# Kernel optimization log

Hardware: AMD Instinct MI355X
Metric: run time of the kernel (lower is better)

Reference implementation:

```python
import jax, jax.numpy as jnp
import numpy as np

D = 256; NH = 8; NL = 4; NP = 4; DFF = 1024
SHAPES = [(100, 100), (50, 50), (25, 25), (13, 13)]
B = 4


def layer_norm(x, g, b, eps=1e-5):
    m = x.mean(-1, keepdims=True)
    v = ((x - m) ** 2).mean(-1, keepdims=True)
    return (x - m) * jax.lax.rsqrt(v + eps) * g + b


def setup_inputs() -> dict:
    key = jax.random.key(0)
    ks = jax.random.split(key, 12)
    Lin = sum(h * w for h, w in SHAPES)  # 13294
    w = lambda k, s: jax.random.normal(k, s, jnp.float32) * 0.02
    return dict(
        src=jax.random.normal(ks[0], (B, Lin, D), jnp.float32),
        pos=0.1 * jax.random.normal(ks[1], (B, Lin, D), jnp.float32),
        reference_points=jax.random.uniform(ks[2], (B, Lin, NL, 2), dtype=jnp.float32),
        spatial_shapes=jnp.array(SHAPES, jnp.int32),
        level_start_index=jnp.array(np.cumsum([0] + [h * w for h, w in SHAPES])[:-1], jnp.int32),
        value_w=w(ks[3], (D, D)), value_b=jnp.zeros((D,), jnp.float32),
        offs_w=w(ks[4], (D, NH * NL * NP * 2)),
        offs_b=0.5 * jax.random.normal(ks[5], (NH * NL * NP * 2,), jnp.float32),
        attn_w=w(ks[6], (D, NH * NL * NP)), attn_b=jnp.zeros((NH * NL * NP,), jnp.float32),
        out_w=w(ks[7], (D, D)), out_b=jnp.zeros((D,), jnp.float32),
        ln1_g=jnp.ones((D,), jnp.float32), ln1_b=jnp.zeros((D,), jnp.float32),
        ff1_w=w(ks[8], (D, DFF)), ff1_b=jnp.zeros((DFF,), jnp.float32),
        ff2_w=w(ks[9], (DFF, D)), ff2_b=jnp.zeros((D,), jnp.float32),
        ln2_g=jnp.ones((D,), jnp.float32), ln2_b=jnp.zeros((D,), jnp.float32),
    )


def msda(query, value_in, ref, shapes, starts, value_w, value_b, offs_w, offs_b,
         attn_w, attn_b, out_w, out_b):
    Bq, Lq, Dm = query.shape
    dh = Dm // NH
    shapes_np = np.asarray(shapes); starts_np = np.asarray(starts)
    value = (value_in @ value_w + value_b).reshape(Bq, -1, NH, dh)
    offs = (query @ offs_w + offs_b).reshape(Bq, Lq, NH, NL, NP, 2)
    aw = jax.nn.softmax((query @ attn_w + attn_b).reshape(Bq, Lq, NH, NL * NP), axis=-1)
    aw = aw.reshape(Bq, Lq, NH, NL, NP)
    # offset normalizer is (W, H) per level
    normalizer = jnp.stack([shapes[:, 1], shapes[:, 0]], -1).astype(jnp.float32)
    loc = ref[:, :, None, :, None, :] + offs / normalizer[None, None, None, :, None, :]
    out = jnp.zeros((Bq, NH, Lq, dh), jnp.float32)
    for l in range(NL):
        Hl, Wl = int(shapes_np[l, 0]), int(shapes_np[l, 1])
        s = int(starts_np[l])
        v = value[:, s:s + Hl * Wl].transpose(0, 2, 1, 3)  # [B,h,HW,dh]
        x = loc[:, :, :, l, :, 0] * Wl - 0.5  # [B,Lq,h,P], align_corners=False
        y = loc[:, :, :, l, :, 1] * Hl - 0.5
        x0 = jnp.floor(x); y0 = jnp.floor(y)
        dx = x - x0; dy = y - y0
        x0i = x0.astype(jnp.int32); y0i = y0.astype(jnp.int32)
        def gather(ix, iy):
            valid = (ix >= 0) & (ix < Wl) & (iy >= 0) & (iy < Hl)  # zero padding
            idx = jnp.clip(iy, 0, Hl - 1) * Wl + jnp.clip(ix, 0, Wl - 1)
            idx = idx.transpose(0, 2, 1, 3).reshape(Bq, NH, Lq * NP)
            g = jnp.take_along_axis(v, idx[..., None], axis=2).reshape(Bq, NH, Lq, NP, dh)
            return g * valid.transpose(0, 2, 1, 3)[..., None]
        dxh = dx.transpose(0, 2, 1, 3)[..., None]
        dyh = dy.transpose(0, 2, 1, 3)[..., None]
        sampled = (gather(x0i, y0i) * (1 - dxh) * (1 - dyh)
                   + gather(x0i + 1, y0i) * dxh * (1 - dyh)
                   + gather(x0i, y0i + 1) * (1 - dxh) * dyh
                   + gather(x0i + 1, y0i + 1) * dxh * dyh)  # [B,h,Lq,P,dh]
        awl = aw[:, :, :, l].transpose(0, 2, 1, 3)[..., None]  # [B,h,Lq,P,1]
        out = out + (sampled * awl).sum(3)
    out = out.transpose(0, 2, 1, 3).reshape(Bq, Lq, Dm)
    return out @ out_w + out_b


def reference(src, pos, reference_points, spatial_shapes, level_start_index,
              value_w, value_b, offs_w, offs_b, attn_w, attn_b, out_w, out_b,
              ln1_g, ln1_b, ff1_w, ff1_b, ff2_w, ff2_b, ln2_g, ln2_b):
    # src = with_pos_embed(src, pos): NOTE this module uses (src + pos) as BOTH query and value
    q = src + pos
    src2 = msda(q, q, reference_points, spatial_shapes, level_start_index,
                value_w, value_b, offs_w, offs_b, attn_w, attn_b, out_w, out_b)
    x = layer_norm(q + src2, ln1_g, ln1_b)  # dropout is identity at eval
    ff = jnp.maximum(x @ ff1_w + ff1_b, 0.0) @ ff2_w + ff2_b
    return layer_norm(x + ff, ln2_g, ln2_b)
```

## Files before the change

kernel.cpp:

```cpp
#include <hip/hip_runtime.h>
#include <hip/hip_bf16.h>

#define B_    4
#define LIN   13294
#define M_    (B_*LIN)
#define D_    256
#define NH_   8
#define NL_   4
#define NP_   4
#define DFF_  1024

typedef __bf16 bf16;
typedef __attribute__((ext_vector_type(8))) __bf16 bfrag8;
typedef __attribute__((ext_vector_type(4))) __bf16 bf16x4;
typedef __attribute__((ext_vector_type(4))) float facc4;

__global__ __launch_bounds__(256) void make_q(const float* __restrict__ src,
                                              const float* __restrict__ pos,
                                              float* __restrict__ q,
                                              bf16* __restrict__ qb, int n4) {
  int i = blockIdx.x * 256 + threadIdx.x;
  if (i >= n4) return;
  float4 s = ((const float4*)src)[i];
  float4 p = ((const float4*)pos)[i];
  float4 v = {s.x + p.x, s.y + p.y, s.z + p.z, s.w + p.w};
  ((float4*)q)[i] = v;
  bf16 t4[4] = {(bf16)v.x, (bf16)v.y, (bf16)v.z, (bf16)v.w};
  ((uint2*)qb)[i] = *(uint2*)t4;
}

__global__ __launch_bounds__(256) void prep_weights(
    const float* __restrict__ vw, const float* __restrict__ ow,
    const float* __restrict__ aw, const float* __restrict__ outw,
    const float* __restrict__ f1w, const float* __restrict__ f2w,
    const float* __restrict__ ob, const float* __restrict__ ab,
    bf16* __restrict__ vwt, bf16* __restrict__ oawt, bf16* __restrict__ outwt,
    bf16* __restrict__ f1wt, bf16* __restrict__ f2wt, float* __restrict__ oabias) {
  int seg = blockIdx.y;
  int idx = blockIdx.x * 256 + threadIdx.x;
  if (seg == 6) {
    if (idx < 256) oabias[idx] = ob[idx];
    else if (idx < 384) oabias[idx] = ab[idx - 256];
    return;
  }
  const float* W; bf16* Wt; int K, N;
  switch (seg) {
    case 0: W = vw;   Wt = vwt;          K = 256;  N = 256;  break;
    case 1: W = ow;   Wt = oawt;         K = 256;  N = 256;  break;
    case 2: W = aw;   Wt = oawt + 65536; K = 256;  N = 128;  break;
    case 3: W = outw; Wt = outwt;        K = 256;  N = 256;  break;
    case 4: W = f1w;  Wt = f1wt;         K = 256;  N = 1024; break;
    default: W = f2w; Wt = f2wt;         K = 1024; N = 256;  break;
  }
  if (idx < K * N) {
    int n = idx / K, k = idx - n * K;
    Wt[idx] = (bf16)W[k * N + n];
  }
}

template<bool RELU>
__global__ __launch_bounds__(256) void gemm_kernel(
    const bf16* __restrict__ A, const bf16* __restrict__ Bt,
    const float* __restrict__ bias, bf16* __restrict__ C,
    int Mdim, int K, int N) {
  __shared__ __align__(16) bf16 As[64][72];
  __shared__ __align__(16) bf16 Bs[64][72];
  int m0 = blockIdx.x * 64;
  int n0 = blockIdx.y * 64;
  int t = threadIdx.x;
  int wave = t >> 6, lane = t & 63;
  int ln = lane & 15, quad = lane >> 4;

  facc4 acc[4];
  facc4 z = {0.f, 0.f, 0.f, 0.f};
  for (int r = 0; r < 4; r++) acc[r] = z;

  for (int k0 = 0; k0 < K; k0 += 64) {
    __syncthreads();
    #pragma unroll
    for (int i = 0; i < 2; i++) {
      int idx = t + i * 256;
      int row = idx >> 3, kc = (idx & 7) * 8;
      int ag = min(m0 + row, Mdim - 1);
      *(uint4*)&As[row][kc] = *(const uint4*)&A[(size_t)ag * K + k0 + kc];
      *(uint4*)&Bs[row][kc] = *(const uint4*)&Bt[(size_t)(n0 + row) * K + k0 + kc];
    }
    __syncthreads();
    #pragma unroll
    for (int kk = 0; kk < 64; kk += 32) {
      bfrag8 bfr = *(const bfrag8*)&Bs[16 * wave + ln][kk + quad * 8];
      #pragma unroll
      for (int r = 0; r < 4; r++) {
        bfrag8 afr = *(const bfrag8*)&As[r * 16 + ln][kk + quad * 8];
        acc[r] = __builtin_amdgcn_mfma_f32_16x16x32_bf16(afr, bfr, acc[r], 0, 0, 0);
      }
    }
  }
  int col = n0 + wave * 16 + ln;
  float bv = bias[col];
  #pragma unroll
  for (int r = 0; r < 4; r++) {
    #pragma unroll
    for (int reg = 0; reg < 4; reg++) {
      int row = m0 + r * 16 + quad * 4 + reg;
      if (row < Mdim) {
        float v = acc[r][reg] + bv;
        if (RELU) v = fmaxf(v, 0.f);
        C[(size_t)row * N + col] = (bf16)v;
      }
    }
  }
}

__global__ __launch_bounds__(256) void msda_sample(
    const bf16* __restrict__ value,
    const bf16* __restrict__ OA,
    const float* __restrict__ ref,
    bf16* __restrict__ sampled) {
  int gw = (blockIdx.x * 256 + threadIdx.x) >> 6;
  int lane = threadIdx.x & 63;
  int m = gw >> 3, h = gw & 7;
  if (m >= M_) return;
  int b = m / LIN;
  int p = lane >> 2, cg = lane & 3;
  int l = p >> 2, pt = p & 3;
  int Wl = (l == 0) ? 100 : (l == 1) ? 50 : (l == 2) ? 25 : 13;
  int Hl = Wl;
  int st = (l == 0) ? 0 : (l == 1) ? 10000 : (l == 2) ? 12500 : 13125;

  float logit = (float)OA[(size_t)m * 384 + 256 + h * 16 + p];
  float mx = logit;
  #pragma unroll
  for (int msk = 4; msk < 64; msk <<= 1) mx = fmaxf(mx, __shfl_xor(mx, msk));
  float e = __expf(logit - mx);
  float se = e;
  #pragma unroll
  for (int msk = 4; msk < 64; msk <<= 1) se += __shfl_xor(se, msk);
  float w = e / se;

  float rx = ref[((size_t)m * 4 + l) * 2 + 0];
  float ry = ref[((size_t)m * 4 + l) * 2 + 1];
  float ox = (float)OA[(size_t)m * 384 + ((h * 4 + l) * 4 + pt) * 2 + 0];
  float oy = (float)OA[(size_t)m * 384 + ((h * 4 + l) * 4 + pt) * 2 + 1];
  float x = rx * (float)Wl + ox - 0.5f;
  float y = ry * (float)Hl + oy - 0.5f;
  float x0f = floorf(x), y0f = floorf(y);
  float dx = x - x0f, dy = y - y0f;
  int x0 = (int)x0f, y0 = (int)y0f;

  float acc[8];
  #pragma unroll
  for (int j = 0; j < 8; j++) acc[j] = 0.f;

  size_t vbase = ((size_t)(b * LIN + st)) * 256 + h * 32 + cg * 8;
  #pragma unroll
  for (int c = 0; c < 4; c++) {
    int cx = c & 1, cy = c >> 1;
    int xi = x0 + cx, yi = y0 + cy;
    bool valid = (xi >= 0) && (xi < Wl) && (yi >= 0) && (yi < Hl);
    int xc = min(max(xi, 0), Wl - 1);
    int yc = min(max(yi, 0), Hl - 1);
    float cw = (cx ? dx : 1.f - dx) * (cy ? dy : 1.f - dy);
    cw = valid ? cw : 0.f;
    bfrag8 vv = *(const bfrag8*)(value + vbase + (size_t)(yc * Wl + xc) * 256);
    #pragma unroll
    for (int j = 0; j < 8; j++) acc[j] += cw * (float)vv[j];
  }
  #pragma unroll
  for (int j = 0; j < 8; j++) acc[j] *= w;
  #pragma unroll
  for (int msk = 4; msk < 64; msk <<= 1) {
    #pragma unroll
    for (int j = 0; j < 8; j++) acc[j] += __shfl_xor(acc[j], msk);
  }
  if (p == 0) {
    bf16 o8[8];
    #pragma unroll
    for (int j = 0; j < 8; j++) o8[j] = (bf16)acc[j];
    *(uint4*)(sampled + (size_t)m * 256 + h * 32 + cg * 8) = *(uint4*)o8;
  }
}

__device__ inline float4 load4f(const float* p) { return *(const float4*)p; }
__device__ inline float4 load4f(const bf16* p) {
  bf16x4 v = *(const bf16x4*)p;
  float4 r = {(float)v[0], (float)v[1], (float)v[2], (float)v[3]};
  return r;
}
template<typename RT>
__global__ __launch_bounds__(256) void ln_kernel(
    const bf16* __restrict__ a, const RT* __restrict__ res,
    const float* __restrict__ g, const float* __restrict__ beta,
    float* __restrict__ out_f, bf16* __restrict__ out_b, int Mdim) {
  int wave = threadIdx.x >> 6, lane = threadIdx.x & 63;
  int row = blockIdx.x * 4 + wave;
  if (row >= Mdim) return;
  size_t base = (size_t)row * 256 + lane * 4;
  float4 av = load4f(a + base);
  float4 rv = load4f(res + base);
  float4 v = {av.x + rv.x, av.y + rv.y, av.z + rv.z, av.w + rv.w};
  float s = v.x + v.y + v.z + v.w;
  #pragma unroll
  for (int msk = 1; msk < 64; msk <<= 1) s += __shfl_xor(s, msk);
  float mean = s * (1.f / 256.f);
  float4 d = {v.x - mean, v.y - mean, v.z - mean, v.w - mean};
  float sq = d.x * d.x + d.y * d.y + d.z * d.z + d.w * d.w;
  #pragma unroll
  for (int msk = 1; msk < 64; msk <<= 1) sq += __shfl_xor(sq, msk);
  float inv = rsqrtf(sq * (1.f / 256.f) + 1e-5f);
  float4 gv = *(const float4*)(g + lane * 4);
  float4 bv = *(const float4*)(beta + lane * 4);
  float4 y = {d.x * inv * gv.x + bv.x, d.y * inv * gv.y + bv.y,
              d.z * inv * gv.z + bv.z, d.w * inv * gv.w + bv.w};
  if (out_f) *(float4*)(out_f + base) = y;
  if (out_b) {
    bf16 t4[4] = {(bf16)y.x, (bf16)y.y, (bf16)y.z, (bf16)y.w};
    *(uint2*)(out_b + base) = *(uint2*)t4;
  }
}

extern "C" void kernel_launch(void* const* d_in, const int* in_sizes, int n_in,
                              void* d_out, int out_size, void* d_ws, size_t ws_size,
                              hipStream_t stream) {
  const float* src     = (const float*)d_in[0];
  const float* pos     = (const float*)d_in[1];
  const float* refpts  = (const float*)d_in[2];
  const float* value_w = (const float*)d_in[5];
  const float* value_b = (const float*)d_in[6];
  const float* offs_w  = (const float*)d_in[7];
  const float* offs_b  = (const float*)d_in[8];
  const float* attn_w  = (const float*)d_in[9];
  const float* attn_b  = (const float*)d_in[10];
  const float* out_w   = (const float*)d_in[11];
  const float* out_b   = (const float*)d_in[12];
  const float* ln1_g   = (const float*)d_in[13];
  const float* ln1_b   = (const float*)d_in[14];
  const float* ff1_w   = (const float*)d_in[15];
  const float* ff1_b   = (const float*)d_in[16];
  const float* ff2_w   = (const float*)d_in[17];
  const float* ff2_b   = (const float*)d_in[18];
  const float* ln2_g   = (const float*)d_in[19];
  const float* ln2_b   = (const float*)d_in[20];

  char* ws = (char*)d_ws;
  size_t off = 0;
  auto take = [&](size_t bytes) -> char* {
    char* pp = ws + off;
    off += (bytes + 255) & ~(size_t)255;
    return pp;
  };
  float* q      = (float*)take((size_t)M_ * 256 * 4);
  size_t szQB   = (size_t)M_ * 256 * 2;
  size_t szOA   = (size_t)M_ * 384 * 2;
  char* R       = take(szQB * 3 + szOA);
  bf16* qb      = (bf16*)R;
  bf16* valueb  = (bf16*)(R + szQB);
  bf16* OA      = (bf16*)(R + 2 * szQB);
  bf16* sampled = (bf16*)(R + 2 * szQB + szOA);
  bf16* hb      = (bf16*)R;
  bf16* tmp     = (bf16*)take(szQB);
  bf16* x       = (bf16*)take(szQB);
  bf16* vwt     = (bf16*)take(65536 * 2);
  bf16* oawt    = (bf16*)take(98304 * 2);
  bf16* outwt   = (bf16*)take(65536 * 2);
  bf16* f1wt    = (bf16*)take(262144 * 2);
  bf16* f2wt    = (bf16*)take(262144 * 2);
  float* oabias = (float*)take(384 * 4);
  (void)ws_size; (void)in_sizes; (void)n_in; (void)out_size;

  int n4 = M_ * 256 / 4;
  make_q<<<dim3((n4 + 255) / 256), dim3(256), 0, stream>>>(src, pos, q, qb, n4);
  prep_weights<<<dim3(1024, 7), dim3(256), 0, stream>>>(
      value_w, offs_w, attn_w, out_w, ff1_w, ff2_w, offs_b, attn_b,
      vwt, oawt, outwt, f1wt, f2wt, oabias);

  dim3 blk(256);
  int mt = (M_ + 63) / 64;
  gemm_kernel<false><<<dim3(mt, 4), blk, 0, stream>>>(qb, vwt, value_b, valueb, M_, 256, 256);
  gemm_kernel<false><<<dim3(mt, 6), blk, 0, stream>>>(qb, oawt, oabias, OA, M_, 256, 384);
  msda_sample<<<dim3(M_ * 2), blk, 0, stream>>>(valueb, OA, refpts, sampled);
  gemm_kernel<false><<<dim3(mt, 4), blk, 0, stream>>>(sampled, outwt, out_b, tmp, M_, 256, 256);
  ln_kernel<float><<<dim3((M_ + 3) / 4), blk, 0, stream>>>(tmp, q, ln1_g, ln1_b, nullptr, x, M_);
  gemm_kernel<true><<<dim3(mt, 16), blk, 0, stream>>>(x, f1wt, ff1_b, hb, M_, 256, 1024);
  gemm_kernel<false><<<dim3(mt, 4), blk, 0, stream>>>(hb, f2wt, ff2_b, tmp, M_, 1024, 256);
  ln_kernel<bf16><<<dim3((M_ + 3) / 4), blk, 0, stream>>>(tmp, x, ln2_g, ln2_b, (float*)d_out, nullptr, M_);
}
```

Measured before the change: 661.3 us.

## Use 128x128 GEMM tiles with direct-to-LDS loads and rework MSDA reduction

```diff
diff --git a/kernel.cpp b/kernel.cpp
--- a/kernel.cpp
+++ b/kernel.cpp
@@ -11,9 +11,11 @@
 #define DFF_  1024
 
 typedef __bf16 bf16;
+typedef unsigned int uint;
 typedef __attribute__((ext_vector_type(8))) __bf16 bfrag8;
 typedef __attribute__((ext_vector_type(4))) __bf16 bf16x4;
 typedef __attribute__((ext_vector_type(4))) float facc4;
+typedef __attribute__((ext_vector_type(2))) float f32x2;
 
 __global__ __launch_bounds__(256) void make_q(const float* __restrict__ src,
                                               const float* __restrict__ pos,
@@ -58,55 +60,95 @@
   }
 }
 
+__device__ __forceinline__ void gload16(const void* g, void* l) {
+  __builtin_amdgcn_global_load_lds(
+      (const __attribute__((address_space(1))) uint*)g,
+      (__attribute__((address_space(3))) uint*)l, 16, 0, 0);
+}
+
 template<bool RELU>
-__global__ __launch_bounds__(256) void gemm_kernel(
+__global__ __launch_bounds__(256) void gemm128(
     const bf16* __restrict__ A, const bf16* __restrict__ Bt,
     const float* __restrict__ bias, bf16* __restrict__ C,
     int Mdim, int K, int N) {
-  __shared__ __align__(16) bf16 As[64][72];
-  __shared__ __align__(16) bf16 Bs[64][72];
-  int m0 = blockIdx.x * 64;
-  int n0 = blockIdx.y * 64;
-  int t = threadIdx.x;
-  int wave = t >> 6, lane = t & 63;
-  int ln = lane & 15, quad = lane >> 4;
-
-  facc4 acc[4];
+  __shared__ __align__(16) bf16 As[128 * 64];
+  __shared__ __align__(16) bf16 Bs[128 * 64];
+  const int t = threadIdx.x, wave = t >> 6, lane = t & 63;
+  const int m0 = blockIdx.x * 128, n0 = blockIdx.y * 128;
+  const int wr = wave >> 1, wc = wave & 1;
+  const int ln = lane & 15, quad = lane >> 4;
+  const int sr = lane >> 3, cc = lane & 7;
+  const int gcol = (cc ^ sr) * 8;
+
+  const bf16* aptr[4]; const bf16* bptr[4];
+  bf16* alds[4]; bf16* blds[4];
+  #pragma unroll
+  for (int ii = 0; ii < 4; ii++) {
+    int i = wave * 4 + ii;
+    int arow = min(m0 + i * 8 + sr, Mdim - 1);
+    aptr[ii] = A + (size_t)arow * K + gcol;
+    bptr[ii] = Bt + (size_t)(n0 + i * 8 + sr) * K + gcol;
+    alds[ii] = As + i * 512;
+    blds[ii] = Bs + i * 512;
+  }
+  int a_off[2][4], b_off[2][4];
+  #pragma unroll
+  for (int ks = 0; ks < 2; ks++) {
+    int gc = ks * 4 + quad;
+    #pragma unroll
+    for (int rt = 0; rt < 4; rt++) {
+      int ra = wr * 64 + rt * 16 + ln;
+      int rb = wc * 64 + rt * 16 + ln;
+      a_off[ks][rt] = ra * 128 + ((gc ^ (ra & 7)) * 16);
+      b_off[ks][rt] = rb * 128 + ((gc ^ (rb & 7)) * 16);
+    }
+  }
+
+  facc4 acc[4][4];
   facc4 z = {0.f, 0.f, 0.f, 0.f};
-  for (int r = 0; r < 4; r++) acc[r] = z;
+  #pragma unroll
+  for (int rt = 0; rt < 4; rt++)
+    #pragma unroll
+    for (int ct = 0; ct < 4; ct++) acc[rt][ct] = z;
 
   for (int k0 = 0; k0 < K; k0 += 64) {
     __syncthreads();
     #pragma unroll
-    for (int i = 0; i < 2; i++) {
-      int idx = t + i * 256;
-      int row = idx >> 3, kc = (idx & 7) * 8;
-      int ag = min(m0 + row, Mdim - 1);
-      *(uint4*)&As[row][kc] = *(const uint4*)&A[(size_t)ag * K + k0 + kc];
-      *(uint4*)&Bs[row][kc] = *(const uint4*)&Bt[(size_t)(n0 + row) * K + k0 + kc];
+    for (int ii = 0; ii < 4; ii++) gload16(aptr[ii] + k0, alds[ii]);
+    #pragma unroll
+    for (int ii = 0; ii < 4; ii++) gload16(bptr[ii] + k0, blds[ii]);
+    __syncthreads();
+    #pragma unroll
+    for (int ks = 0; ks < 2; ks++) {
+      bfrag8 afr[4], bfr[4];
+      #pragma unroll
+      for (int ct = 0; ct < 4; ct++)
+        bfr[ct] = *(const bfrag8*)((const char*)Bs + b_off[ks][ct]);
+      #pragma unroll
+      for (int rt = 0; rt < 4; rt++)
+        afr[rt] = *(const bfrag8*)((const char*)As + a_off[ks][rt]);
+      #pragma unroll
+      for (int rt = 0; rt < 4; rt++)
+        #pragma unroll
+        for (int ct = 0; ct < 4; ct++)
+          acc[rt][ct] = __builtin_amdgcn_mfma_f32_16x16x32_bf16(afr[rt], bfr[ct], acc[rt][ct], 0, 0, 0);
     }
-    __syncthreads();
-    #pragma unroll
-    for (int kk = 0; kk < 64; kk += 32) {
-      bfrag8 bfr = *(const bfrag8*)&Bs[16 * wave + ln][kk + quad * 8];
+  }
+
+  #pragma unroll
+  for (int ct = 0; ct < 4; ct++) {
+    int col = n0 + wc * 64 + ct * 16 + ln;
+    float bv = bias[col];
+    #pragma unroll
+    for (int rt = 0; rt < 4; rt++) {
       #pragma unroll
-      for (int r = 0; r < 4; r++) {
-        bfrag8 afr = *(const bfrag8*)&As[r * 16 + ln][kk + quad * 8];
-        acc[r] = __builtin_amdgcn_mfma_f32_16x16x32_bf16(afr, bfr, acc[r], 0, 0, 0);
-      }
-    }
-  }
-  int col = n0 + wave * 16 + ln;
-  float bv = bias[col];
-  #pragma unroll
-  for (int r = 0; r < 4; r++) {
-    #pragma unroll
-    for (int reg = 0; reg < 4; reg++) {
-      int row = m0 + r * 16 + quad * 4 + reg;
-      if (row < Mdim) {
-        float v = acc[r][reg] + bv;
-        if (RELU) v = fmaxf(v, 0.f);
-        C[(size_t)row * N + col] = (bf16)v;
+      for (int reg = 0; reg < 4; reg++) {
+        int row = m0 + wr * 64 + rt * 16 + quad * 4 + reg;
+        if (row < Mdim) {
+          float v = acc[rt][ct][reg] + bv;
+          if (RELU) v = fmaxf(v, 0.f);
+          C[(size_t)row * N + col] = (bf16)v;
+        }
       }
     }
   }
@@ -147,37 +189,62 @@
   float x0f = floorf(x), y0f = floorf(y);
   float dx = x - x0f, dy = y - y0f;
   int x0 = (int)x0f, y0 = (int)y0f;
-
-  float acc[8];
-  #pragma unroll
-  for (int j = 0; j < 8; j++) acc[j] = 0.f;
+  float wx1 = 1.f - dx, wy1 = 1.f - dy;
+
+  f32x2 acc2[4];
+  #pragma unroll
+  for (int t = 0; t < 4; t++) acc2[t] = (f32x2){0.f, 0.f};
 
   size_t vbase = ((size_t)(b * LIN + st)) * 256 + h * 32 + cg * 8;
   #pragma unroll
   for (int c = 0; c < 4; c++) {
     int cx = c & 1, cy = c >> 1;
     int xi = x0 + cx, yi = y0 + cy;
-    bool valid = (xi >= 0) && (xi < Wl) && (yi >= 0) && (yi < Hl);
+    bool valid = (xi >= 0) & (xi < Wl) & (yi >= 0) & (yi < Hl);
     int xc = min(max(xi, 0), Wl - 1);
     int yc = min(max(yi, 0), Hl - 1);
-    float cw = (cx ? dx : 1.f - dx) * (cy ? dy : 1.f - dy);
+    float cw = (cx ? dx : wx1) * (cy ? dy : wy1) * w;
     cw = valid ? cw : 0.f;
-    bfrag8 vv = *(const bfrag8*)(value + vbase + (size_t)(yc * Wl + xc) * 256);
-    #pragma unroll
-    for (int j = 0; j < 8; j++) acc[j] += cw * (float)vv[j];
-  }
-  #pragma unroll
-  for (int j = 0; j < 8; j++) acc[j] *= w;
-  #pragma unroll
-  for (int msk = 4; msk < 64; msk <<= 1) {
-    #pragma unroll
-    for (int j = 0; j < 8; j++) acc[j] += __shfl_xor(acc[j], msk);
-  }
-  if (p == 0) {
-    bf16 o8[8];
-    #pragma unroll
-    for (int j = 0; j < 8; j++) o8[j] = (bf16)acc[j];
-    *(uint4*)(sampled + (size_t)m * 256 + h * 32 + cg * 8) = *(uint4*)o8;
+    uint off = (uint)(yc * Wl + xc) * 256u;
+    const uint4 vv = *(const uint4*)(value + vbase + off);
+    f32x2 cw2 = {cw, cw};
+    f32x2 v0 = {__uint_as_float(vv.x << 16), __uint_as_float(vv.x & 0xffff0000u)};
+    f32x2 v1 = {__uint_as_float(vv.y << 16), __uint_as_float(vv.y & 0xffff0000u)};
+    f32x2 v2 = {__uint_as_float(vv.z << 16), __uint_as_float(vv.z & 0xffff0000u)};
+    f32x2 v3 = {__uint_as_float(vv.w << 16), __uint_as_float(vv.w & 0xffff0000u)};
+    acc2[0] = cw2 * v0 + acc2[0];
+    acc2[1] = cw2 * v1 + acc2[1];
+    acc2[2] = cw2 * v2 + acc2[2];
+    acc2[3] = cw2 * v3 + acc2[3];
+  }
+
+  int sel = (lane >> 2) & 1;
+  f32x2 sA0 = sel ? acc2[0] : acc2[2];
+  f32x2 sA1 = sel ? acc2[1] : acc2[3];
+  f32x2 kA0 = sel ? acc2[2] : acc2[0];
+  f32x2 kA1 = sel ? acc2[3] : acc2[1];
+  f32x2 rA0, rA1;
+  rA0.x = __shfl_xor(sA0.x, 4); rA0.y = __shfl_xor(sA0.y, 4);
+  rA1.x = __shfl_xor(sA1.x, 4); rA1.y = __shfl_xor(sA1.y, 4);
+  kA0 += rA0; kA1 += rA1;
+
+  int sel2 = (lane >> 3) & 1;
+  f32x2 sB = sel2 ? kA0 : kA1;
+  f32x2 kB = sel2 ? kA1 : kA0;
+  f32x2 rB;
+  rB.x = __shfl_xor(sB.x, 8); rB.y = __shfl_xor(sB.y, 8);
+  kB += rB;
+
+  int sel3 = (lane >> 4) & 1;
+  float sC = sel3 ? kB.x : kB.y;
+  float kC = sel3 ? kB.y : kB.x;
+  kC += __shfl_xor(sC, 16);
+
+  float v = kC + __shfl_xor(kC, 32);
+
+  if (lane < 32) {
+    int c = cg * 8 + ((lane >> 2) & 1) * 4 + ((lane >> 3) & 1) * 2 + ((lane >> 4) & 1);
+    sampled[(size_t)m * 256 + h * 32 + c] = (bf16)v;
   }
 }
 
@@ -275,13 +342,13 @@
       vwt, oawt, outwt, f1wt, f2wt, oabias);
 
   dim3 blk(256);
-  int mt = (M_ + 63) / 64;
-  gemm_kernel<false><<<dim3(mt, 4), blk, 0, stream>>>(qb, vwt, value_b, valueb, M_, 256, 256);
-  gemm_kernel<false><<<dim3(mt, 6), blk, 0, stream>>>(qb, oawt, oabias, OA, M_, 256, 384);
+  int mt = (M_ + 127) / 128;
+  gemm128<false><<<dim3(mt, 2), blk, 0, stream>>>(qb, vwt, value_b, valueb, M_, 256, 256);
+  gemm128<false><<<dim3(mt, 3), blk, 0, stream>>>(qb, oawt, oabias, OA, M_, 256, 384);
   msda_sample<<<dim3(M_ * 2), blk, 0, stream>>>(valueb, OA, refpts, sampled);
-  gemm_kernel<false><<<dim3(mt, 4), blk, 0, stream>>>(sampled, outwt, out_b, tmp, M_, 256, 256);
+  gemm128<false><<<dim3(mt, 2), blk, 0, stream>>>(sampled, outwt, out_b, tmp, M_, 256, 256);
   ln_kernel<float><<<dim3((M_ + 3) / 4), blk, 0, stream>>>(tmp, q, ln1_g, ln1_b, nullptr, x, M_);
-  gemm_kernel<true><<<dim3(mt, 16), blk, 0, stream>>>(x, f1wt, ff1_b, hb, M_, 256, 1024);
-  gemm_kernel<false><<<dim3(mt, 4), blk, 0, stream>>>(hb, f2wt, ff2_b, tmp, M_, 1024, 256);
+  gemm128<true><<<dim3(mt, 8), blk, 0, stream>>>(x, f1wt, ff1_b, hb, M_, 256, 1024);
+  gemm128<false><<<dim3(mt, 2), blk, 0, stream>>>(hb, f2wt, ff2_b, tmp, M_, 1024, 256);
   ln_kernel<bf16><<<dim3((M_ + 3) / 4), blk, 0, stream>>>(tmp, x, ln2_g, ln2_b, (float*)d_out, nullptr, M_);
 }
```

Result: no change. 672.7 us (+1.7%).
